# Kernel optimization log

Hardware: AMD Instinct MI355X
Metric: run time of the kernel (lower is better)

The kernel has to match this reference:

```python
import jax, jax.numpy as jnp
import numpy as np

NUM_CLASSES = 60
NUM_HEADS = 8
TOP_M = 20
LN_EPS = 1e-5
NUM_LAYERS = 2


def setup_inputs() -> dict:
    key = jax.random.key(0)
    ks = jax.random.split(key, 13)
    D = 256  # feature_dim
    S = 72   # seq_len
    BNC = 32 * NUM_CLASSES  # batch * num_classes = 1920
    s = lambda k, shape, sc=0.02: jax.random.normal(k, shape, dtype=jnp.float32) * sc
    return {
        "reweighted_features": jax.random.normal(ks[0], (BNC, D, S), dtype=jnp.float32),
        "pos_embed": s(ks[1], (1, S, D)),
        # per-layer weights stacked on leading axis (L=2); Linear stored as (in, out)
        "qkv_w": s(ks[2], (NUM_LAYERS, D, 3 * D)),
        "qkv_b": jnp.zeros((NUM_LAYERS, 3 * D), dtype=jnp.float32),
        "proj_w": s(ks[3], (NUM_LAYERS, D, D)),
        "proj_b": jnp.zeros((NUM_LAYERS, D), dtype=jnp.float32),
        "ln_g": jnp.ones((NUM_LAYERS, D), dtype=jnp.float32),
        "ln_b": jnp.zeros((NUM_LAYERS, D), dtype=jnp.float32),
        "cls_w1": s(ks[4], (D, D // 2)),
        "cls_b1": jnp.zeros((D // 2,), dtype=jnp.float32),
        "cls_w2": s(ks[5], (D // 2, 1)),
        "cls_b2": jnp.zeros((1,), dtype=jnp.float32),
    }


def _layer_norm(x, g, b):
    mu = jnp.mean(x, axis=-1, keepdims=True)
    var = jnp.mean(jnp.square(x - mu), axis=-1, keepdims=True)
    return (x - mu) * jax.lax.rsqrt(var + LN_EPS) * g + b


def _topm_attention(x, qkv_w, qkv_b, proj_w, proj_b):
    B, N, C = x.shape
    hd = C // NUM_HEADS
    scale = hd ** -0.5
    qkv = (x @ qkv_w + qkv_b).reshape(B, N, 3, NUM_HEADS, hd)
    qkv = qkv.transpose(2, 0, 3, 1, 4)  # (3, B, H, N, hd)
    q, k, v = qkv[0], qkv[1], qkv[2]
    attn = jnp.einsum("bhnd,bhmd->bhnm", q, k) * scale  # (B, H, N, N)
    if TOP_M < N:
        # keep only the top-m scores per query row (ties negligible for random floats)
        topv = jax.lax.top_k(attn, TOP_M)[0]
        thr = topv[..., -1:]
        attn = jnp.where(attn >= thr, attn, -jnp.inf)
    p = jax.nn.softmax(attn, axis=-1)
    out = jnp.einsum("bhnm,bhmd->bhnd", p, v)
    out = out.transpose(0, 2, 1, 3).reshape(B, N, C)
    return out @ proj_w + proj_b


def reference(reweighted_features, pos_embed, qkv_w, qkv_b, proj_w, proj_b,
              ln_g, ln_b, cls_w1, cls_b1, cls_w2, cls_b2):
    BNC, D, S = reweighted_features.shape
    batch = BNC // NUM_CLASSES
    x = reweighted_features.transpose(0, 2, 1) + pos_embed  # (BNC, S, D)
    for i in range(NUM_LAYERS):
        x = x + _topm_attention(x, qkv_w[i], qkv_b[i], proj_w[i], proj_b[i])
        x = _layer_norm(x, ln_g[i], ln_b[i])
    x = x.mean(axis=1)  # (BNC, D)
    x = x.reshape(batch, NUM_CLASSES, D)
    h = jax.nn.relu(x @ cls_w1 + cls_b1)
    logits = (h @ cls_w2 + cls_b2)[..., 0]  # (batch, NUM_CLASSES)
    return logits
```

## Files before the change

kernel.cpp:

```cpp
#include <hip/hip_runtime.h>

#define NTOK 72
#define TOPM 20
#define GSEQ 4

typedef __attribute__((ext_vector_type(8))) short s8v;
typedef __attribute__((ext_vector_type(4))) float f4v;
typedef __attribute__((ext_vector_type(4))) unsigned short u16x4;

#define MFMA16(a, b, c) __builtin_amdgcn_mfma_f32_16x16x32_bf16((a), (b), (c), 0, 0, 0)

__device__ __forceinline__ unsigned short f2bf(float f) {
  unsigned int u = __float_as_uint(f);
  unsigned int r = (u + 0x7FFFu + ((u >> 16) & 1u)) >> 16;
  return (unsigned short)r;
}
__device__ __forceinline__ float bf2f(unsigned short s) {
  return __uint_as_float(((unsigned int)s) << 16);
}

__global__ void pack_w(const float* __restrict__ qkv_w, const float* __restrict__ proj_w,
                       const float* __restrict__ pos,
                       unsigned short* __restrict__ wq, unsigned short* __restrict__ wp,
                       unsigned short* __restrict__ posb) {
  int idx = blockIdx.x * 256 + threadIdx.x;
  if (idx < 2 * 768 * 256) {
    int k = idx & 255; int rest = idx >> 8; int j = rest % 768; int l = rest / 768;
    int h = j / 96, j96 = j - h * 96;
    int which = j96 >> 5, d = j96 & 31;
    wq[idx] = f2bf(qkv_w[(l * 256 + k) * 768 + which * 256 + h * 32 + d]);
  }
  if (idx < 2 * 256 * 256) {
    int k = idx & 255, n = (idx >> 8) & 255, l = idx >> 16;
    wp[idx] = f2bf(proj_w[(l * 256 + k) * 256 + n]);
  }
  if (idx < 72 * 256) posb[idx] = f2bf(pos[idx]);
}

__global__ __launch_bounds__(512, 2)
void k_qkv(const float* __restrict__ rf, const unsigned short* __restrict__ posb,
           unsigned short* __restrict__ xb,
           const unsigned short* __restrict__ wq,
           const float* __restrict__ qkv_b,
           unsigned short* __restrict__ qkvbuf,
           int layer, int b0)
{
  __shared__ __align__(16) unsigned short xs[80 * 264];
  __shared__ __align__(16) unsigned short st[256 * 72];
  const int tid = threadIdx.x, w = tid >> 6, l = tid & 63, q4 = l >> 4, l15 = l & 15;

  for (int i = tid; i < 80 * 264 / 2; i += 512) ((unsigned int*)xs)[i] = 0u;
  __syncthreads();

  const unsigned short* wqB = wq + (size_t)layer * 768 * 256;

  for (int g = 0; g < GSEQ; ++g) {
    const int b = blockIdx.x * GSEQ + g + b0;
    if (layer == 0) {
      const float* rfb = rf + (size_t)b * 18432;
      for (int i = tid; i < 18432; i += 512) {
        int c = i / 72, n = i - c * 72;
        float v = __builtin_nontemporal_load(rfb + i);
        xs[n * 264 + c] = f2bf(v + bf2f(posb[n * 256 + c]));
      }
    } else {
      const unsigned short* xbb = xb + (size_t)b * 18432;
      for (int i = tid; i < 2304; i += 512) {
        int n = i >> 5, c8 = (i & 31) << 3;
        s8v v = __builtin_nontemporal_load((const s8v*)(xbb + n * 256 + c8));
        *(s8v*)(xs + n * 264 + c8) = v;
      }
    }
    __syncthreads();
    if (layer == 0) {
      unsigned short* xbb = xb + (size_t)b * 18432;
      for (int i = tid; i < 2304; i += 512) {
        int n = i >> 5, c8 = (i & 31) << 3;
        __builtin_nontemporal_store(*(const s8v*)(xs + n * 264 + c8), (s8v*)(xbb + n * 256 + c8));
      }
    }

    unsigned short* qkvS = qkvbuf + (size_t)(b - b0) * 55296;
    for (int pass = 0; pass < 3; ++pass) {
      int jb[2], j768b[2], hh[2], j96b[2], whg[2];
      #pragma unroll
      for (int jj = 0; jj < 2; ++jj) {
        jb[jj] = (w + 8 * jj) * 16;
        j768b[jj] = pass * 256 + jb[jj];
        hh[jj] = j768b[jj] / 96;
        j96b[jj] = j768b[jj] - hh[jj] * 96;
        whg[jj] = j96b[jj] >> 5;
      }
      f4v acc[2][5];
      #pragma unroll
      for (int jj = 0; jj < 2; ++jj)
        #pragma unroll
        for (int mt = 0; mt < 5; ++mt) acc[jj][mt] = (f4v){0, 0, 0, 0};
      for (int kk = 0; kk < 8; ++kk) {
        int k0 = kk * 32 + q4 * 8;
        s8v a[5];
        #pragma unroll
        for (int mt = 0; mt < 5; ++mt) a[mt] = *(const s8v*)(xs + (mt * 16 + l15) * 264 + k0);
        #pragma unroll
        for (int jj = 0; jj < 2; ++jj) {
          s8v bw = *(const s8v*)(wqB + (j768b[jj] + l15) * 256 + k0);
          if (whg[jj] < 2) {
            #pragma unroll
            for (int mt = 0; mt < 5; ++mt) acc[jj][mt] = MFMA16(bw, a[mt], acc[jj][mt]);
          } else {
            #pragma unroll
            for (int mt = 0; mt < 5; ++mt) acc[jj][mt] = MFMA16(a[mt], bw, acc[jj][mt]);
          }
        }
      }
      #pragma unroll
      for (int jj = 0; jj < 2; ++jj) {
        int gg = jb[jj] >> 5;
        unsigned short* stg = st + gg * 2304;
        if (whg[jj] < 2) {
          int dloc = (j96b[jj] & 31) + q4 * 4;
          float scl = (whg[jj] == 0) ? 0.17677669529663687f : 1.0f;
          float bv[4];
          #pragma unroll
          for (int r = 0; r < 4; ++r)
            bv[r] = qkv_b[layer * 768 + whg[jj] * 256 + hh[jj] * 32 + dloc + r];
          #pragma unroll
          for (int mt = 0; mt < 5; ++mt) {
            int tok = mt * 16 + l15;
            if (tok < NTOK) {
              u16x4 pk;
              #pragma unroll
              for (int r = 0; r < 4; ++r) pk[r] = f2bf((acc[jj][mt][r] + bv[r]) * scl);
              *(u16x4*)(stg + tok * 32 + dloc) = pk;
            }
          }
        } else {
          int d = (j96b[jj] & 31) + l15;
          float bv = qkv_b[layer * 768 + 512 + hh[jj] * 32 + d];
          #pragma unroll
          for (int mt = 0; mt < 5; ++mt) {
            int tok0 = mt * 16 + q4 * 4;
            if (tok0 < NTOK) {
              u16x4 pk;
              #pragma unroll
              for (int r = 0; r < 4; ++r) pk[r] = f2bf(acc[jj][mt][r] + bv);
              *(u16x4*)(stg + d * 72 + tok0) = pk;
            }
          }
        }
      }
      __syncthreads();
      unsigned short* dst = qkvS + pass * 18432;
      for (int i = tid; i < 2304; i += 512)
        __builtin_nontemporal_store(*(const s8v*)(st + i * 8), (s8v*)(dst + i * 8));
      __syncthreads();
    }
  }
}

#define SP_S 104
__global__ __launch_bounds__(256, 4)
void k_attn(const unsigned short* __restrict__ qkvbuf, unsigned short* __restrict__ ohbuf,
            int b0)
{
  __shared__ __align__(16) unsigned short qs[80 * 40];
  __shared__ __align__(16) unsigned short ks[80 * 40];
  __shared__ __align__(16) unsigned short vt[32 * SP_S];
  __shared__ __align__(16) unsigned short sp[80 * SP_S];
  unsigned short* ostage = qs;
  const int tid = threadIdx.x, w = tid >> 6, l = tid & 63, q4 = l >> 4, l15 = l & 15;
  const int bh = blockIdx.x;
  const int b = (bh >> 3) + b0, h = bh & 7;
  const unsigned short* qgq = qkvbuf + (size_t)(bh >> 3) * 55296 + (size_t)h * 6912;
  const unsigned short* qgk = qgq + 2304;
  const unsigned short* qgv = qgq + 4608;

  for (int i = tid; i < 160; i += 256) ((unsigned int*)(qs + 72 * 40))[i] = 0u;
  for (int i = tid; i < 160; i += 256) ((unsigned int*)(ks + 72 * 40))[i] = 0u;
  for (int i = tid; i < 512; i += 256) {
    int d = i >> 4, c = (i & 15) << 1;
    *(unsigned int*)(vt + d * SP_S + 72 + c) = 0u;
  }
  for (int i = tid; i < 960; i += 256) {
    int rr = i / 12, c = (i % 12) << 1;
    *(unsigned int*)(sp + rr * SP_S + 80 + c) = 0u;
  }
  for (int i = tid; i < 288; i += 256) {
    int tok = i >> 2, d8 = (i & 3) << 3;
    s8v v = __builtin_nontemporal_load((const s8v*)(qgq + tok * 32 + d8));
    *(s8v*)(qs + tok * 40 + d8) = v;
  }
  for (int i = tid; i < 288; i += 256) {
    int tok = i >> 2, d8 = (i & 3) << 3;
    s8v v = __builtin_nontemporal_load((const s8v*)(qgk + tok * 32 + d8));
    *(s8v*)(ks + tok * 40 + d8) = v;
  }
  for (int i = tid; i < 288; i += 256) {
    int d = i / 9, t8 = (i - d * 9) << 3;
    s8v v = __builtin_nontemporal_load((const s8v*)(qgv + d * 72 + t8));
    *(s8v*)(vt + d * SP_S + t8) = v;
  }
  __syncthreads();

  for (int t = w; t < 25; t += 4) {
    int mt = t / 5, kt = t - mt * 5;
    s8v a  = *(const s8v*)(qs + (mt * 16 + l15) * 40 + q4 * 8);
    s8v bf = *(const s8v*)(ks + (kt * 16 + l15) * 40 + q4 * 8);
    f4v c = MFMA16(a, bf, ((f4v){0, 0, 0, 0}));
    int rowb = mt * 16 + q4 * 4, col = kt * 16 + l15;
    #pragma unroll
    for (int r = 0; r < 4; ++r) sp[(rowb + r) * SP_S + col] = f2bf(c[r]);
  }
  __syncthreads();

  const int rowsh = l & 56;
  for (int rp = 0; rp < 3; ++rp) {
    int row = rp * 32 + w * 8 + (l >> 3);
    if (row < NTOK) {
      int sub = l & 7;
      unsigned short* rowp = sp + row * SP_S;
      s8v raw = *(const s8v*)(rowp + sub * 8);
      unsigned short uv[9];
      #pragma unroll
      for (int i = 0; i < 8; ++i) uv[i] = (unsigned short)raw[i];
      uv[8] = rowp[64 + sub];
      float vf[9]; unsigned int key[9];
      #pragma unroll
      for (int i = 0; i < 9; ++i) {
        unsigned int s = uv[i];
        vf[i] = bf2f((unsigned short)s);
        key[i] = s ^ ((s >> 15) ? 0xFFFFu : 0x8000u);
      }
      unsigned int thr = 0u;
      for (int bit = 15; bit >= 0; --bit) {
        unsigned int cand = thr | (1u << bit);
        int cnt = 0;
        #pragma unroll
        for (int i = 0; i < 9; ++i) {
          unsigned long long m = __ballot(key[i] >= cand);
          cnt += __popc((unsigned int)(m >> rowsh) & 0xffu);
        }
        if (cnt >= TOPM) thr = cand;
      }
      float mx = vf[0];
      #pragma unroll
      for (int i = 1; i < 9; ++i) mx = fmaxf(mx, vf[i]);
      mx = fmaxf(mx, __shfl_xor(mx, 1));
      mx = fmaxf(mx, __shfl_xor(mx, 2));
      mx = fmaxf(mx, __shfl_xor(mx, 4));
      float ssum = 0.f;
      #pragma unroll
      for (int i = 0; i < 9; ++i) {
        float e = (key[i] >= thr) ? __expf(vf[i] - mx) : 0.f;
        vf[i] = e; ssum += e;
      }
      ssum += __shfl_xor(ssum, 1);
      ssum += __shfl_xor(ssum, 2);
      ssum += __shfl_xor(ssum, 4);
      float inv = 1.f / ssum;
      s8v pout;
      #pragma unroll
      for (int i = 0; i < 8; ++i) pout[i] = (short)f2bf(vf[i] * inv);
      *(s8v*)(rowp + sub * 8) = pout;
      rowp[64 + sub] = f2bf(vf[8] * inv);
    }
  }
  __syncthreads();

  for (int t = w; t < 10; t += 4) {
    int mt = t >> 1, dt = t & 1;
    f4v acc = (f4v){0, 0, 0, 0};
    #pragma unroll
    for (int kk = 0; kk < 3; ++kk) {
      int k0 = kk * 32 + q4 * 8;
      s8v a  = *(const s8v*)(sp + (mt * 16 + l15) * SP_S + k0);
      s8v bf = *(const s8v*)(vt + (dt * 16 + l15) * SP_S + k0);
      acc = MFMA16(a, bf, acc);
    }
    int rowb = mt * 16 + q4 * 4, d = dt * 16 + l15;
    #pragma unroll
    for (int r = 0; r < 4; ++r) ostage[(rowb + r) * 32 + d] = f2bf(acc[r]);
  }
  __syncthreads();

  unsigned short* ohb = ohbuf + (size_t)b * 18432 + h * 32;
  for (int i = tid; i < 288; i += 256) {
    int tok = i >> 2, c8 = (i & 3) << 3;
    __builtin_nontemporal_store(*(const s8v*)(ostage + tok * 32 + c8), (s8v*)(ohb + tok * 256 + c8));
  }
}

__global__ __launch_bounds__(512, 2)
void k_proj(const unsigned short* __restrict__ ohbuf, const unsigned short* __restrict__ wp,
            const float* __restrict__ proj_b, const float* __restrict__ ln_g,
            const float* __restrict__ ln_b,
            unsigned short* __restrict__ xb,
            const float* __restrict__ w1, const float* __restrict__ b1,
            const float* __restrict__ w2, const float* __restrict__ b2,
            float* __restrict__ out, int layer, int last)
{
  __shared__ __align__(16) unsigned short os[80 * 264];
  __shared__ float red[160];
  __shared__ float mbufs[GSEQ][256];
  __shared__ float hb[GSEQ][128];
  const int tid = threadIdx.x, w = tid >> 6, l = tid & 63, q4 = l >> 4, l15 = l & 15;

  for (int i = tid; i < 80 * 264 / 2; i += 512) ((unsigned int*)os)[i] = 0u;
  for (int i = tid; i < GSEQ * 256; i += 512) ((float*)mbufs)[i] = 0.f;
  if (tid < GSEQ * 128) ((float*)hb)[tid] = 0.f;
  __syncthreads();

  const unsigned short* wpB = wp + (size_t)layer * 65536;
  const int c0 = w * 32 + l15, c1 = c0 + 16;
  const float pb0 = proj_b[layer * 256 + c0], pb1 = proj_b[layer * 256 + c1];
  const float g0 = ln_g[layer * 256 + c0], g1 = ln_g[layer * 256 + c1];
  const float be0 = ln_b[layer * 256 + c0], be1 = ln_b[layer * 256 + c1];

  for (int g = 0; g < GSEQ; ++g) {
    const int b = blockIdx.x * GSEQ + g;
    const unsigned short* ohb = ohbuf + (size_t)b * 18432;
    for (int i = tid; i < 2304; i += 512) {
      int n = i >> 5, c8 = (i & 31) << 3;
      s8v v = __builtin_nontemporal_load((const s8v*)(ohb + n * 256 + c8));
      *(s8v*)(os + n * 264 + c8) = v;
    }
    if (tid < 160) red[tid] = 0.f;
    __syncthreads();

    f4v acc[5][2];
    #pragma unroll
    for (int mt = 0; mt < 5; ++mt) { acc[mt][0] = (f4v){0,0,0,0}; acc[mt][1] = (f4v){0,0,0,0}; }
    for (int kk = 0; kk < 8; ++kk) {
      int k0 = kk * 32 + q4 * 8;
      s8v a[5];
      #pragma unroll
      for (int mt = 0; mt < 5; ++mt) a[mt] = *(const s8v*)(os + (mt * 16 + l15) * 264 + k0);
      #pragma unroll
      for (int j = 0; j < 2; ++j) {
        int nrow = w * 32 + j * 16 + l15;
        s8v bf = *(const s8v*)(wpB + nrow * 256 + k0);
        #pragma unroll
        for (int mt = 0; mt < 5; ++mt) acc[mt][j] = MFMA16(a[mt], bf, acc[mt][j]);
      }
    }

    const unsigned short* xbb = xb + (size_t)b * 18432;
    #pragma unroll
    for (int mt = 0; mt < 5; ++mt) {
      #pragma unroll
      for (int r = 0; r < 4; ++r) {
        int row = mt * 16 + q4 * 4 + r;
        float z0 = 0.f, z1 = 0.f;
        if (row < NTOK) {
          z0 = bf2f(xbb[row * 256 + c0]) + acc[mt][0][r] + pb0;
          z1 = bf2f(xbb[row * 256 + c1]) + acc[mt][1][r] + pb1;
        }
        acc[mt][0][r] = z0; acc[mt][1][r] = z1;
        float s1 = z0 + z1, s2 = z0 * z0 + z1 * z1;
        s1 += __shfl_xor(s1, 1); s2 += __shfl_xor(s2, 1);
        s1 += __shfl_xor(s1, 2); s2 += __shfl_xor(s2, 2);
        s1 += __shfl_xor(s1, 4); s2 += __shfl_xor(s2, 4);
        s1 += __shfl_xor(s1, 8); s2 += __shfl_xor(s2, 8);
        if (l15 == 0 && row < NTOK) {
          atomicAdd(&red[row * 2], s1);
          atomicAdd(&red[row * 2 + 1], s2);
        }
      }
    }
    __syncthreads();

    float msum0 = 0.f, msum1 = 0.f;
    #pragma unroll
    for (int mt = 0; mt < 5; ++mt) {
      #pragma unroll
      for (int r = 0; r < 4; ++r) {
        int row = mt * 16 + q4 * 4 + r;
        if (row < NTOK) {
          float mu = red[row * 2] * (1.f / 256.f);
          float var = red[row * 2 + 1] * (1.f / 256.f) - mu * mu;
          float rstd = rsqrtf(var + 1e-5f);
          float o0 = (acc[mt][0][r] - mu) * rstd * g0 + be0;
          float o1 = (acc[mt][1][r] - mu) * rstd * g1 + be1;
          if (!last) {
            os[row * 264 + c0] = f2bf(o0);
            os[row * 264 + c1] = f2bf(o1);
          } else {
            msum0 += o0; msum1 += o1;
          }
        }
      }
    }
    if (last) {
      atomicAdd(&mbufs[g][c0], msum0);
      atomicAdd(&mbufs[g][c1], msum1);
    }
    __syncthreads();
    if (!last) {
      unsigned short* xbw = xb + (size_t)b * 18432;
      for (int i = tid; i < 2304; i += 512) {
        int n = i >> 5, c8 = (i & 31) << 3;
        __builtin_nontemporal_store(*(const s8v*)(os + n * 264 + c8), (s8v*)(xbw + n * 256 + c8));
      }
    }
    __syncthreads();
  }

  if (last) {
    {
      int col = tid & 127, kq = tid >> 7;
      float sums[GSEQ];
      #pragma unroll
      for (int g = 0; g < GSEQ; ++g) sums[g] = 0.f;
      for (int k = kq * 64; k < kq * 64 + 64; ++k) {
        float wv = w1[k * 128 + col] * (1.f / 72.f);
        #pragma unroll
        for (int g = 0; g < GSEQ; ++g) sums[g] += mbufs[g][k] * wv;
      }
      #pragma unroll
      for (int g = 0; g < GSEQ; ++g) atomicAdd(&hb[g][col], sums[g]);
    }
    __syncthreads();
    if (w == 0) {
      #pragma unroll
      for (int g = 0; g < GSEQ; ++g) {
        float h0 = fmaxf(hb[g][l] + b1[l], 0.f);
        float h1 = fmaxf(hb[g][l + 64] + b1[l + 64], 0.f);
        float p = h0 * w2[l] + h1 * w2[l + 64];
        p += __shfl_xor(p, 1);  p += __shfl_xor(p, 2);  p += __shfl_xor(p, 4);
        p += __shfl_xor(p, 8);  p += __shfl_xor(p, 16); p += __shfl_xor(p, 32);
        if (l == 0) out[blockIdx.x * GSEQ + g] = p + b2[0];
      }
    }
  }
}

extern "C" void kernel_launch(void* const* d_in, const int* in_sizes, int n_in,
                              void* d_out, int out_size, void* d_ws, size_t ws_size,
                              hipStream_t stream) {
  const float* rf    = (const float*)d_in[0];
  const float* pos   = (const float*)d_in[1];
  const float* qkvw  = (const float*)d_in[2];
  const float* qkvb  = (const float*)d_in[3];
  const float* projw = (const float*)d_in[4];
  const float* projb = (const float*)d_in[5];
  const float* lng   = (const float*)d_in[6];
  const float* lnb   = (const float*)d_in[7];
  const float* w1    = (const float*)d_in[8];
  const float* b1    = (const float*)d_in[9];
  const float* w2    = (const float*)d_in[10];
  const float* b2    = (const float*)d_in[11];
  float* out = (float*)d_out;

  unsigned short* wq   = (unsigned short*)d_ws;
  unsigned short* wp   = wq + 393216;
  unsigned short* posb = wp + 131072;
  unsigned short* xb   = posb + 18432;
  unsigned short* oh   = xb + 35389440;
  unsigned short* qkv  = oh + 35389440;

  const size_t fixed_bytes = (size_t)(393216 + 131072 + 18432 + 35389440 + 35389440) * 2;
  const size_t qkv_bytes   = (size_t)1920 * 768 * 72 * 2;
  int nc = 1;
  while (nc < 8 && fixed_bytes + qkv_bytes / nc > ws_size) nc *= 2;
  const int bc = 1920 / nc;

  hipLaunchKernelGGL(pack_w, dim3(1536), dim3(256), 0, stream, qkvw, projw, pos, wq, wp, posb);
  for (int layer = 0; layer < 2; ++layer) {
    for (int c = 0; c < nc; ++c) {
      int b0 = c * bc;
      hipLaunchKernelGGL(k_qkv, dim3(bc / GSEQ), dim3(512), 0, stream,
                         rf, posb, xb, wq, qkvb, qkv, layer, b0);
      hipLaunchKernelGGL(k_attn, dim3(bc * 8), dim3(256), 0, stream, qkv, oh, b0);
    }
    hipLaunchKernelGGL(k_proj, dim3(1920 / GSEQ), dim3(512), 0, stream,
                       oh, wp, projb, lng, lnb, xb, w1, b1, w2, b2, out,
                       layer, layer == 1 ? 1 : 0);
  }
}
```

Baseline: 1.409 ms.

## Vectorize layer-0 input load, drop nontemporal hints and padding zero-fills

The layer-0 input load now reads four floats per thread and adds a pre-transposed bf16 positional embedding, instead of scalar loads with strided posb lookups. Every nontemporal load and store on the intermediate buffers becomes a plain access, so those buffers can stay resident in L2/MALL between kernels. Several zero-fills of shared-memory padding rows are removed along with their barriers. The risk is that the padding rows (tokens 72-79) are no longer cleared, so MFMA tiles may read stale shared memory in rows whose outputs are discarded; garbage there could still leak in if it contains NaN or Inf.

```diff
diff --git a/kernel.cpp b/kernel.cpp
--- a/kernel.cpp
+++ b/kernel.cpp
@@ -22,7 +22,7 @@
 __global__ void pack_w(const float* __restrict__ qkv_w, const float* __restrict__ proj_w,
                        const float* __restrict__ pos,
                        unsigned short* __restrict__ wq, unsigned short* __restrict__ wp,
-                       unsigned short* __restrict__ posb) {
+                       unsigned short* __restrict__ posT) {
   int idx = blockIdx.x * 256 + threadIdx.x;
   if (idx < 2 * 768 * 256) {
     int k = idx & 255; int rest = idx >> 8; int j = rest % 768; int l = rest / 768;
@@ -34,11 +34,14 @@
     int k = idx & 255, n = (idx >> 8) & 255, l = idx >> 16;
     wp[idx] = f2bf(proj_w[(l * 256 + k) * 256 + n]);
   }
-  if (idx < 72 * 256) posb[idx] = f2bf(pos[idx]);
+  if (idx < 72 * 256) {
+    int c = idx / 72, n = idx - c * 72;
+    posT[idx] = f2bf(pos[n * 256 + c]);
+  }
 }
 
 __global__ __launch_bounds__(512, 2)
-void k_qkv(const float* __restrict__ rf, const unsigned short* __restrict__ posb,
+void k_qkv(const float* __restrict__ rf, const unsigned short* __restrict__ posT,
            unsigned short* __restrict__ xb,
            const unsigned short* __restrict__ wq,
            const float* __restrict__ qkv_b,
@@ -49,26 +52,25 @@
   __shared__ __align__(16) unsigned short st[256 * 72];
   const int tid = threadIdx.x, w = tid >> 6, l = tid & 63, q4 = l >> 4, l15 = l & 15;
 
-  for (int i = tid; i < 80 * 264 / 2; i += 512) ((unsigned int*)xs)[i] = 0u;
-  __syncthreads();
-
   const unsigned short* wqB = wq + (size_t)layer * 768 * 256;
 
   for (int g = 0; g < GSEQ; ++g) {
     const int b = blockIdx.x * GSEQ + g + b0;
     if (layer == 0) {
-      const float* rfb = rf + (size_t)b * 18432;
-      for (int i = tid; i < 18432; i += 512) {
-        int c = i / 72, n = i - c * 72;
-        float v = __builtin_nontemporal_load(rfb + i);
-        xs[n * 264 + c] = f2bf(v + bf2f(posb[n * 256 + c]));
+      const f4v* rfb4 = (const f4v*)(rf + (size_t)b * 18432);
+      for (int i = tid; i < 4608; i += 512) {
+        int c = i / 18, n0 = (i - c * 18) * 4;
+        f4v v = __builtin_nontemporal_load(rfb4 + i);
+        u16x4 p = *(const u16x4*)(posT + i * 4);
+        #pragma unroll
+        for (int r = 0; r < 4; ++r)
+          xs[(n0 + r) * 264 + c] = f2bf(v[r] + bf2f(p[r]));
       }
     } else {
       const unsigned short* xbb = xb + (size_t)b * 18432;
       for (int i = tid; i < 2304; i += 512) {
         int n = i >> 5, c8 = (i & 31) << 3;
-        s8v v = __builtin_nontemporal_load((const s8v*)(xbb + n * 256 + c8));
-        *(s8v*)(xs + n * 264 + c8) = v;
+        *(s8v*)(xs + n * 264 + c8) = *(const s8v*)(xbb + n * 256 + c8);
       }
     }
     __syncthreads();
@@ -76,7 +78,7 @@
       unsigned short* xbb = xb + (size_t)b * 18432;
       for (int i = tid; i < 2304; i += 512) {
         int n = i >> 5, c8 = (i & 31) << 3;
-        __builtin_nontemporal_store(*(const s8v*)(xs + n * 264 + c8), (s8v*)(xbb + n * 256 + c8));
+        *(s8v*)(xbb + n * 256 + c8) = *(const s8v*)(xs + n * 264 + c8);
       }
     }
 
@@ -152,7 +154,7 @@
       __syncthreads();
       unsigned short* dst = qkvS + pass * 18432;
       for (int i = tid; i < 2304; i += 512)
-        __builtin_nontemporal_store(*(const s8v*)(st + i * 8), (s8v*)(dst + i * 8));
+        *(s8v*)(dst + i * 8) = *(const s8v*)(st + i * 8);
       __syncthreads();
     }
   }
@@ -175,7 +177,6 @@
   const unsigned short* qgk = qgq + 2304;
   const unsigned short* qgv = qgq + 4608;
 
-  for (int i = tid; i < 160; i += 256) ((unsigned int*)(qs + 72 * 40))[i] = 0u;
   for (int i = tid; i < 160; i += 256) ((unsigned int*)(ks + 72 * 40))[i] = 0u;
   for (int i = tid; i < 512; i += 256) {
     int d = i >> 4, c = (i & 15) << 1;
@@ -187,18 +188,15 @@
   }
   for (int i = tid; i < 288; i += 256) {
     int tok = i >> 2, d8 = (i & 3) << 3;
-    s8v v = __builtin_nontemporal_load((const s8v*)(qgq + tok * 32 + d8));
-    *(s8v*)(qs + tok * 40 + d8) = v;
+    *(s8v*)(qs + tok * 40 + d8) = *(const s8v*)(qgq + tok * 32 + d8);
   }
   for (int i = tid; i < 288; i += 256) {
     int tok = i >> 2, d8 = (i & 3) << 3;
-    s8v v = __builtin_nontemporal_load((const s8v*)(qgk + tok * 32 + d8));
-    *(s8v*)(ks + tok * 40 + d8) = v;
+    *(s8v*)(ks + tok * 40 + d8) = *(const s8v*)(qgk + tok * 32 + d8);
   }
   for (int i = tid; i < 288; i += 256) {
     int d = i / 9, t8 = (i - d * 9) << 3;
-    s8v v = __builtin_nontemporal_load((const s8v*)(qgv + d * 72 + t8));
-    *(s8v*)(vt + d * SP_S + t8) = v;
+    *(s8v*)(vt + d * SP_S + t8) = *(const s8v*)(qgv + d * 72 + t8);
   }
   __syncthreads();
 
@@ -286,7 +284,7 @@
   unsigned short* ohb = ohbuf + (size_t)b * 18432 + h * 32;
   for (int i = tid; i < 288; i += 256) {
     int tok = i >> 2, c8 = (i & 3) << 3;
-    __builtin_nontemporal_store(*(const s8v*)(ostage + tok * 32 + c8), (s8v*)(ohb + tok * 256 + c8));
+    *(s8v*)(ohb + tok * 256 + c8) = *(const s8v*)(ostage + tok * 32 + c8);
   }
 }
 
@@ -305,10 +303,8 @@
   __shared__ float hb[GSEQ][128];
   const int tid = threadIdx.x, w = tid >> 6, l = tid & 63, q4 = l >> 4, l15 = l & 15;
 
-  for (int i = tid; i < 80 * 264 / 2; i += 512) ((unsigned int*)os)[i] = 0u;
   for (int i = tid; i < GSEQ * 256; i += 512) ((float*)mbufs)[i] = 0.f;
   if (tid < GSEQ * 128) ((float*)hb)[tid] = 0.f;
-  __syncthreads();
 
   const unsigned short* wpB = wp + (size_t)layer * 65536;
   const int c0 = w * 32 + l15, c1 = c0 + 16;
@@ -321,8 +317,7 @@
     const unsigned short* ohb = ohbuf + (size_t)b * 18432;
     for (int i = tid; i < 2304; i += 512) {
       int n = i >> 5, c8 = (i & 31) << 3;
-      s8v v = __builtin_nontemporal_load((const s8v*)(ohb + n * 256 + c8));
-      *(s8v*)(os + n * 264 + c8) = v;
+      *(s8v*)(os + n * 264 + c8) = *(const s8v*)(ohb + n * 256 + c8);
     }
     if (tid < 160) red[tid] = 0.f;
     __syncthreads();
@@ -399,7 +394,7 @@
       unsigned short* xbw = xb + (size_t)b * 18432;
       for (int i = tid; i < 2304; i += 512) {
         int n = i >> 5, c8 = (i & 31) << 3;
-        __builtin_nontemporal_store(*(const s8v*)(os + n * 264 + c8), (s8v*)(xbw + n * 256 + c8));
+        *(s8v*)(xbw + n * 256 + c8) = *(const s8v*)(os + n * 264 + c8);
       }
     }
     __syncthreads();
@@ -453,8 +448,8 @@
 
   unsigned short* wq   = (unsigned short*)d_ws;
   unsigned short* wp   = wq + 393216;
-  unsigned short* posb = wp + 131072;
-  unsigned short* xb   = posb + 18432;
+  unsigned short* posT = wp + 131072;
+  unsigned short* xb   = posT + 18432;
   unsigned short* oh   = xb + 35389440;
   unsigned short* qkv  = oh + 35389440;
 
@@ -464,12 +459,12 @@
   while (nc < 8 && fixed_bytes + qkv_bytes / nc > ws_size) nc *= 2;
   const int bc = 1920 / nc;
 
-  hipLaunchKernelGGL(pack_w, dim3(1536), dim3(256), 0, stream, qkvw, projw, pos, wq, wp, posb);
+  hipLaunchKernelGGL(pack_w, dim3(1536), dim3(256), 0, stream, qkvw, projw, pos, wq, wp, posT);
   for (int layer = 0; layer < 2; ++layer) {
     for (int c = 0; c < nc; ++c) {
       int b0 = c * bc;
       hipLaunchKernelGGL(k_qkv, dim3(bc / GSEQ), dim3(512), 0, stream,
-                         rf, posb, xb, wq, qkvb, qkv, layer, b0);
+                         rf, posT, xb, wq, qkvb, qkv, layer, b0);
       hipLaunchKernelGGL(k_attn, dim3(bc * 8), dim3(256), 0, stream, qkv, oh, b0);
     }
     hipLaunchKernelGGL(k_proj, dim3(1920 / GSEQ), dim3(512), 0, stream,
```

After: 1.355 ms. 1.04x faster.
